# Optimization experiments

Hardware: AMD Instinct MI355X
Metric: run time of the kernel (lower is better)

## Reference

```python
import jax, jax.numpy as jnp
import numpy as np

B, N, D, V, Y = 4, 4096, 512, 50257, 16000

def setup_inputs() -> dict:
    key = jax.random.key(0)
    ks = jax.random.split(key, 5)
    # token ids in [1, V): avoid pad_id=0 so no attention row is fully -inf
    M_s = jax.random.randint(ks[0], (B, N), 1, V)
    E_v = jax.random.normal(ks[1], (V, D), jnp.float32) * 0.02
    E_y = jax.random.normal(ks[2], (Y, D), jnp.float32) * 0.02
    s = 1.0 / np.sqrt(D)  # kaiming_uniform(a=sqrt(5)) bound for [D,D]
    W_A = jax.random.uniform(ks[3], (D, D), jnp.float32, minval=-s, maxval=s)
    W_O = jax.random.uniform(ks[4], (D, D), jnp.float32, minval=-s, maxval=s)
    gamma = jnp.ones((D,), jnp.float32)
    beta = jnp.zeros((D,), jnp.float32)
    return {"M_s": M_s, "E_v": E_v, "E_y": E_y, "W_A": W_A, "W_O": W_O,
            "gamma": gamma, "beta": beta}

def _layer_norm(x, g, b, eps=1e-5):
    mu = jnp.mean(x, axis=-1, keepdims=True)
    var = jnp.mean(jnp.square(x - mu), axis=-1, keepdims=True)
    return (x - mu) * jax.lax.rsqrt(var + eps) * g + b

def reference(M_s, E_v, E_y, W_A, W_O, gamma, beta):
    # Self-attention branch (v_q=None), dropout in eval mode (identity).
    X = E_v[M_s]                                   # [B, N, D]
    mask = (M_s != 0)                              # [B, N] padding mask
    # logits = (X @ W_A) @ X^T
    logits = jnp.einsum('bnd,de,bme->bnm', X, W_A, X)   # [B, N, N]
    logits = jnp.where(mask[:, None, :], logits, -jnp.inf)
    # positional + causal bias: D = -|i-j| with future (i<j) set to -inf
    i = jnp.arange(N, dtype=jnp.float32)[:, None]
    j = jnp.arange(N, dtype=jnp.float32)[None, :]
    dist = i - j
    bias = jnp.where(dist >= 0, -dist, -jnp.inf)        # [N, N]
    A = jax.nn.softmax(logits + bias, axis=-1)          # [B, N, N]
    Q_c = jnp.einsum('bnm,bmd,de->bne', A, X, W_O)      # [B, N, D]
    H = _layer_norm(Q_c + X, gamma, beta)               # [B, N, D]
    y_logits = jnp.einsum('bnd,yd->bny', H, E_y)        # [B, N, Y]
    return y_logits, A
```

## Files before the change

kernel.cpp:

```cpp
#include <hip/hip_runtime.h>


#define DEVINL __device__ __forceinline__

typedef __attribute__((ext_vector_type(8))) short bf16x8;
typedef __attribute__((ext_vector_type(4))) float f32x4;
typedef unsigned short u16;

#define BB 4
#define NN 4096
#define DD 512
#define YY 16000
#define YPAD 16128
#define ROWS (BB * NN)

DEVINL u16 f2bf(float x) {
  unsigned u = __float_as_uint(x);
  return (u16)((u + 0x7fffu + ((u >> 16) & 1u)) >> 16);
}

DEVINL float bf2f(u16 h) { return __uint_as_float((unsigned)h << 16); }

DEVINL void gload16(const void* g, void* l) {
  __builtin_amdgcn_global_load_lds(
      (const __attribute__((address_space(1))) void*)g,
      (__attribute__((address_space(3))) void*)l, 16, 0, 0);
}

DEVINL void zero_acc(f32x4 acc[4][4]) {
#pragma unroll
  for (int m = 0; m < 4; ++m)
#pragma unroll
    for (int n = 0; n < 4; ++n) {
      acc[m][n][0] = 0.f; acc[m][n][1] = 0.f;
      acc[m][n][2] = 0.f; acc[m][n][3] = 0.f;
    }
}

DEVINL void gemm_bt_core(const u16* __restrict__ A, int lda,
                         const u16* __restrict__ Bm, int ldb, int ksteps,
                         u16* sA, u16* sB, f32x4 acc[4][4], int tid) {
  const int lane = tid & 63, w = tid >> 6;
  const int wr = (w >> 1) * 64, wc = (w & 1) * 64;
  const int c0 = w * 128 + lane, c1 = c0 + 64;
  const u16* gA0 = A + (size_t)(c0 >> 2) * lda + (c0 & 3) * 8;
  const u16* gA1 = A + (size_t)(c1 >> 2) * lda + (c1 & 3) * 8;
  const u16* gB0 = Bm + (size_t)(c0 >> 2) * ldb + (c0 & 3) * 8;
  const u16* gB1 = Bm + (size_t)(c1 >> 2) * ldb + (c1 & 3) * 8;
  u16* lA0 = sA + w * 1024;  u16* lA1 = lA0 + 512;
  u16* lB0 = sB + w * 1024;  u16* lB1 = lB0 + 512;
  const int fr = lane & 15, fk = (lane >> 4) * 8;

  for (int kt = 0; kt < ksteps; ++kt) {
    __syncthreads();
    gload16(gA0 + kt * 32, lA0);
    gload16(gA1 + kt * 32, lA1);
    gload16(gB0 + kt * 32, lB0);
    gload16(gB1 + kt * 32, lB1);
    __syncthreads();
    bf16x8 af[4], bfv[4];
#pragma unroll
    for (int m = 0; m < 4; ++m)
      af[m] = *(const bf16x8*)(sA + (wr + m * 16 + fr) * 32 + fk);
#pragma unroll
    for (int n = 0; n < 4; ++n)
      bfv[n] = *(const bf16x8*)(sB + (wc + n * 16 + fr) * 32 + fk);
#pragma unroll
    for (int m = 0; m < 4; ++m)
#pragma unroll
      for (int n = 0; n < 4; ++n)
        acc[m][n] = __builtin_amdgcn_mfma_f32_16x16x32_bf16(af[m], bfv[n],
                                                            acc[m][n], 0, 0, 0);
  }
}

#define C256_STAGE(kt, buf)                                    \
  {                                                            \
    const u16* a0 = Ag + (kt) * 64;                            \
    const u16* b0 = Bg + (kt) * 64;                            \
    u16* Lb = lds + (buf) * 32768;                             \
    gload16(a0 + offE0, Lb + d0);                              \
    gload16(a0 + offE1, Lb + d1);                              \
    gload16(a0 + 65536 + offE0, Lb + 8192 + d0);               \
    gload16(a0 + 65536 + offE1, Lb + 8192 + d1);               \
    gload16(b0 + offE0, Lb + 16384 + d0);                      \
    gload16(b0 + offE1, Lb + 16384 + d1);                      \
    gload16(b0 + 65536 + offE0, Lb + 24576 + d0);              \
    gload16(b0 + 65536 + offE1, Lb + 24576 + d1);              \
  }

DEVINL void core256(const u16* __restrict__ Ag, const u16* __restrict__ Bg,
                    u16* lds, f32x4 (&acc)[8][4], int tid) {
  const int lane = tid & 63, w = tid >> 6;
  const int wm = w >> 2, wn = w & 3;

  int offE0, offE1;
  {
    int q = tid;
    int r = (((q >> 6) >> 1) << 4) | ((q >> 2) & 15);
    int c = (((q >> 6) & 1) << 5) |
            (((q & 3) << 3) ^ (((q >> 5) & 1) << 4) ^ (((q >> 4) & 1) << 3));
    offE0 = r * DD + c;
    q = 512 + tid;
    r = (((q >> 6) >> 1) << 4) | ((q >> 2) & 15);
    c = (((q >> 6) & 1) << 5) |
        (((q & 3) << 3) ^ (((q >> 5) & 1) << 4) ^ (((q >> 4) & 1) << 3));
    offE1 = r * DD + c;
  }
  const int d0 = w * 512, d1 = 4096 + w * 512;

  int x = (lane & 15) * 64 + ((lane >> 4) & 3) * 16;
  int fxu = (x ^ (((x >> 9) & 1) << 5) ^ (((x >> 8) & 1) << 4)) >> 1;

#pragma unroll
  for (int m = 0; m < 8; ++m)
#pragma unroll
    for (int n = 0; n < 4; ++n) {
      acc[m][n][0] = 0.f; acc[m][n][1] = 0.f;
      acc[m][n][2] = 0.f; acc[m][n][3] = 0.f;
    }

  C256_STAGE(0, 0);
  C256_STAGE(1, 1);
  asm volatile("s_waitcnt vmcnt(8)" ::: "memory");
  __syncthreads();

  for (int c = 0; c < 8; ++c) {
    const u16* L = lds + (c & 1) * 32768;
    const u16* pa = L + wm * 8192;
    const u16* pb = L + 16384 + (wn >> 1) * 8192 + (wn & 1) * 4096;
    bf16x8 af[4][2], bf[4][2];
#pragma unroll
    for (int n = 0; n < 2; ++n)
#pragma unroll
      for (int ks = 0; ks < 2; ++ks)
        bf[n][ks] = *(const bf16x8*)(pb + (n * 2 + ks) * 512 + fxu);
#pragma unroll
    for (int m = 0; m < 4; ++m)
#pragma unroll
      for (int ks = 0; ks < 2; ++ks)
        af[m][ks] = *(const bf16x8*)(pa + (m * 2 + ks) * 512 + fxu);
    __builtin_amdgcn_s_setprio(1);
#pragma unroll
    for (int m = 0; m < 4; ++m)
#pragma unroll
      for (int n = 0; n < 2; ++n)
#pragma unroll
        for (int ks = 0; ks < 2; ++ks)
          acc[m][n] = __builtin_amdgcn_mfma_f32_16x16x32_bf16(
              af[m][ks], bf[n][ks], acc[m][n], 0, 0, 0);
    __builtin_amdgcn_s_setprio(0);
#pragma unroll
    for (int n = 2; n < 4; ++n)
#pragma unroll
      for (int ks = 0; ks < 2; ++ks)
        bf[n][ks] = *(const bf16x8*)(pb + (n * 2 + ks) * 512 + fxu);
    __builtin_amdgcn_s_setprio(1);
#pragma unroll
    for (int m = 0; m < 4; ++m)
#pragma unroll
      for (int n = 2; n < 4; ++n)
#pragma unroll
        for (int ks = 0; ks < 2; ++ks)
          acc[m][n] = __builtin_amdgcn_mfma_f32_16x16x32_bf16(
              af[m][ks], bf[n][ks], acc[m][n], 0, 0, 0);
    __builtin_amdgcn_s_setprio(0);
#pragma unroll
    for (int m = 0; m < 4; ++m)
#pragma unroll
      for (int ks = 0; ks < 2; ++ks)
        af[m][ks] = *(const bf16x8*)(pa + ((m + 4) * 2 + ks) * 512 + fxu);
    __builtin_amdgcn_s_setprio(1);
#pragma unroll
    for (int m = 0; m < 4; ++m)
#pragma unroll
      for (int n = 0; n < 2; ++n)
#pragma unroll
        for (int ks = 0; ks < 2; ++ks)
          acc[m + 4][n] = __builtin_amdgcn_mfma_f32_16x16x32_bf16(
              af[m][ks], bf[n][ks], acc[m + 4][n], 0, 0, 0);
#pragma unroll
    for (int m = 0; m < 4; ++m)
#pragma unroll
      for (int n = 2; n < 4; ++n)
#pragma unroll
        for (int ks = 0; ks < 2; ++ks)
          acc[m + 4][n] = __builtin_amdgcn_mfma_f32_16x16x32_bf16(
              af[m][ks], bf[n][ks], acc[m + 4][n], 0, 0, 0);
    __builtin_amdgcn_s_setprio(0);

    __syncthreads();
    if (c < 6) {
      C256_STAGE(c + 2, c & 1);
      asm volatile("s_waitcnt vmcnt(8)" ::: "memory");
    } else if (c == 6) {
      asm volatile("s_waitcnt vmcnt(0)" ::: "memory");
    }
    __syncthreads();
  }
}

__global__ __launch_bounds__(128) void prep_gather(const int* __restrict__ Ms,
                                                   const float* __restrict__ Ev,
                                                   u16* __restrict__ Xb) {
  int row = blockIdx.x, tid = threadIdx.x;
  int tok = Ms[row];
  float4 v = *(const float4*)(Ev + (size_t)tok * DD + tid * 4);
  *(ushort4*)(Xb + (size_t)row * DD + tid * 4) =
      make_ushort4(f2bf(v.x), f2bf(v.y), f2bf(v.z), f2bf(v.w));
}

__global__ __launch_bounds__(256) void prep_wt(const float* __restrict__ W,
                                               u16* __restrict__ Wt) {
  __shared__ u16 t[64][65];
  int dt = blockIdx.x, et = blockIdx.y, tid = threadIdx.x;
#pragma unroll
  for (int p = 0; p < 16; ++p) {
    int e = tid + 256 * p; int r = e >> 6, c = e & 63;
    t[r][c] = f2bf(W[(size_t)(dt * 64 + r) * DD + et * 64 + c]);
  }
  __syncthreads();
#pragma unroll
  for (int p = 0; p < 16; ++p) {
    int e = tid + 256 * p; int r = e >> 6, c = e & 63;
    Wt[(size_t)(et * 64 + r) * DD + dt * 64 + c] = t[c][r];
  }
}

__global__ __launch_bounds__(256) void prep_ey(const float* __restrict__ Ey,
                                               u16* __restrict__ Eyb) {
  size_t i4 = (size_t)blockIdx.x * 256 + threadIdx.x;
  size_t row = i4 >> 7;
  ushort4 h;
  if (row < YY) {
    float4 v = *(const float4*)(Ey + i4 * 4);
    h = make_ushort4(f2bf(v.x), f2bf(v.y), f2bf(v.z), f2bf(v.w));
  } else {
    h = make_ushort4(0, 0, 0, 0);
  }
  *(ushort4*)(Eyb + i4 * 4) = h;
}

__global__ __launch_bounds__(256) void prep_xt(const u16* __restrict__ Xb,
                                               u16* __restrict__ XbT) {
  __shared__ u16 t[64][65];
  int tid = threadIdx.x;
  int nt = blockIdx.x, dt = blockIdx.y, b = blockIdx.z;
  const u16* src = Xb + ((size_t)b * NN + nt * 64) * DD + dt * 64;
#pragma unroll
  for (int p = 0; p < 16; ++p) {
    int e = tid + 256 * p; int r = e >> 6, c = e & 63;
    t[r][c] = src[(size_t)r * DD + c];
  }
  __syncthreads();
  u16* dst = XbT + ((size_t)b * DD + dt * 64) * NN + nt * 64;
#pragma unroll
  for (int p = 0; p < 16; ++p) {
    int e = tid + 256 * p; int r = e >> 6, c = e & 63;
    dst[(size_t)r * NN + c] = t[c][r];
  }
}

__global__ __launch_bounds__(256) void k2_xw(const u16* __restrict__ Xb,
                                             const u16* __restrict__ WAt,
                                             u16* __restrict__ XWb) {
  __shared__ u16 sA[4096], sB[4096];
  f32x4 acc[4][4]; zero_acc(acc);
  int tid = threadIdx.x;
  size_t row0 = (size_t)blockIdx.x * 128, col0 = (size_t)blockIdx.y * 128;
  gemm_bt_core(Xb + row0 * DD, DD, WAt + col0 * DD, DD, DD / 32, sA, sB, acc, tid);
  int lane = tid & 63, w = tid >> 6;
  int wr = (w >> 1) * 64, wc = (w & 1) * 64;
  int cr = (lane >> 4) * 4, cc = lane & 15;
#pragma unroll
  for (int m = 0; m < 4; ++m)
#pragma unroll
    for (int n = 0; n < 4; ++n)
#pragma unroll
      for (int r = 0; r < 4; ++r) {
        size_t gi = row0 + wr + m * 16 + cr + r;
        size_t gj = col0 + wc + n * 16 + cc;
        XWb[gi * DD + gj] = f2bf(acc[m][n][r]);
      }
}

__global__ __launch_bounds__(256) void k3_scores(const u16* __restrict__ XWb,
                                                 const u16* __restrict__ Xb,
                                                 u16* __restrict__ Ebf) {
  int t = blockIdx.x, b = blockIdx.z;
  int ib = (int)((sqrtf(8.f * (float)t + 1.f) - 1.f) * 0.5f);
  while ((ib + 1) * (ib + 2) / 2 <= t) ++ib;
  while (ib * (ib + 1) / 2 > t) --ib;
  int jb = t - ib * (ib + 1) / 2;
  __shared__ u16 sA[4096], sB[4096];
  f32x4 acc[4][4]; zero_acc(acc);
  int tid = threadIdx.x;
  const u16* Ap = XWb + ((size_t)b * NN + ib * 128) * DD;
  const u16* Bp = Xb  + ((size_t)b * NN + jb * 128) * DD;
  gemm_bt_core(Ap, DD, Bp, DD, DD / 32, sA, sB, acc, tid);
  int lane = tid & 63, w = tid >> 6;
  int wr = (w >> 1) * 64, wc = (w & 1) * 64;
  int cr = (lane >> 4) * 4, cc = lane & 15;
  u16* Eb = Ebf + (size_t)b * NN * NN;
#pragma unroll
  for (int m = 0; m < 4; ++m)
#pragma unroll
    for (int n = 0; n < 4; ++n)
#pragma unroll
      for (int r = 0; r < 4; ++r) {
        int i = ib * 128 + wr + m * 16 + cr + r;
        int j = jb * 128 + wc + n * 16 + cc;
        float e = (j > i) ? 0.f : __expf(acc[m][n][r] - (float)(i - j));
        Eb[(size_t)i * NN + j] = f2bf(e);
      }
}

__global__ __launch_bounds__(256) void k4_softmax(const u16* __restrict__ Ebf,
                                                  float* __restrict__ Aout,
                                                  float* __restrict__ invb) {
  __shared__ u16 srow[NN];
  __shared__ float red[4];
  size_t row = blockIdx.x;
  int i = (int)(row & (NN - 1));
  const u16* E = Ebf + row * (size_t)NN;
  float* S = Aout + row * (size_t)NN;
  int len = i + 1, tid = threadIdx.x;
  int padend = (len + 127) & ~127;
  int nc = padend >> 3;
  for (int v = tid; v < nc; v += 256)
    *(uint4*)(srow + v * 8) = *(const uint4*)(E + v * 8);
  __syncthreads();
  float l = 0.f;
  for (int v = tid; v < nc; v += 256) {
    uint4 x = *(const uint4*)(srow + v * 8);
    l += bf2f((u16)(x.x & 0xffff)) + bf2f((u16)(x.x >> 16));
    l += bf2f((u16)(x.y & 0xffff)) + bf2f((u16)(x.y >> 16));
    l += bf2f((u16)(x.z & 0xffff)) + bf2f((u16)(x.z >> 16));
    l += bf2f((u16)(x.w & 0xffff)) + bf2f((u16)(x.w >> 16));
  }
#pragma unroll
  for (int o = 32; o; o >>= 1) l += __shfl_xor(l, o);
  if ((tid & 63) == 0) red[tid >> 6] = l;
  __syncthreads();
  float inv = 1.f / (red[0] + red[1] + red[2] + red[3]);
  if (tid == 0) invb[row] = inv;
  for (int v = tid; v < NN / 4; v += 256) {
    int k = v * 4;
    float4 a = make_float4(0.f, 0.f, 0.f, 0.f);
    if (k < padend) {
      ushort4 e = *(const ushort4*)(srow + k);
      a = make_float4(bf2f(e.x) * inv, bf2f(e.y) * inv,
                      bf2f(e.z) * inv, bf2f(e.w) * inv);
    }
    *(float4*)(S + k) = a;
  }
}

__global__ __launch_bounds__(256) void k5_ax(const u16* __restrict__ Ebf,
                                             const u16* __restrict__ XbT,
                                             const float* __restrict__ invb,
                                             u16* __restrict__ AXb) {
  int u = blockIdx.x;
  int half = u >> 8, v = u & 255;
  int ib = v & 31; if (half) ib = 31 - ib;
  int db = (v >> 5) & 3;
  int b = (half << 1) | (v >> 7);
  __shared__ u16 sA[4096], sB[4096];
  f32x4 acc[4][4]; zero_acc(acc);
  int tid = threadIdx.x;
  const u16* Ap = Ebf + ((size_t)b * NN + ib * 128) * NN;
  const u16* Bp = XbT + ((size_t)b * DD + db * 128) * NN;
  gemm_bt_core(Ap, NN, Bp, NN, (ib + 1) * 4, sA, sB, acc, tid);
  int lane = tid & 63, w = tid >> 6;
  int wr = (w >> 1) * 64, wc = (w & 1) * 64;
  int cr = (lane >> 4) * 4, cc = lane & 15;
#pragma unroll
  for (int m = 0; m < 4; ++m)
#pragma unroll
    for (int r = 0; r < 4; ++r) {
      int i = ib * 128 + wr + m * 16 + cr + r;
      float sc = invb[(size_t)b * NN + i];
#pragma unroll
      for (int n = 0; n < 4; ++n) {
        int d = db * 128 + wc + n * 16 + cc;
        AXb[((size_t)b * NN + i) * DD + d] = f2bf(acc[m][n][r] * sc);
      }
    }
}

__global__ __launch_bounds__(256) void k6_qc(const u16* __restrict__ AXb,
                                             const u16* __restrict__ WOt,
                                             float* __restrict__ Qc32) {
  __shared__ u16 sA[4096], sB[4096];
  f32x4 acc[4][4]; zero_acc(acc);
  int tid = threadIdx.x;
  size_t row0 = (size_t)blockIdx.x * 128, col0 = (size_t)blockIdx.y * 128;
  gemm_bt_core(AXb + row0 * DD, DD, WOt + col0 * DD, DD, DD / 32, sA, sB, acc, tid);
  int lane = tid & 63, w = tid >> 6;
  int wr = (w >> 1) * 64, wc = (w & 1) * 64;
  int cr = (lane >> 4) * 4, cc = lane & 15;
#pragma unroll
  for (int m = 0; m < 4; ++m)
#pragma unroll
    for (int n = 0; n < 4; ++n)
#pragma unroll
      for (int r = 0; r < 4; ++r) {
        size_t gi = row0 + wr + m * 16 + cr + r;
        size_t gj = col0 + wc + n * 16 + cc;
        Qc32[gi * DD + gj] = acc[m][n][r];
      }
}

__global__ __launch_bounds__(128) void k6b_ln(const float* __restrict__ Qc,
                                              const u16* __restrict__ Xb,
                                              const float* __restrict__ gamma,
                                              const float* __restrict__ beta,
                                              u16* __restrict__ Hb) {
  int row = blockIdx.x, tid = threadIdx.x;
  float4 q = *(const float4*)(Qc + (size_t)row * DD + tid * 4);
  ushort4 xu = *(const ushort4*)(Xb + (size_t)row * DD + tid * 4);
  float v0 = q.x + bf2f(xu.x), v1 = q.y + bf2f(xu.y);
  float v2 = q.z + bf2f(xu.z), v3 = q.w + bf2f(xu.w);
  float s = v0 + v1 + v2 + v3;
  float s2 = v0 * v0 + v1 * v1 + v2 * v2 + v3 * v3;
#pragma unroll
  for (int o = 32; o; o >>= 1) { s += __shfl_xor(s, o); s2 += __shfl_xor(s2, o); }
  __shared__ float r1[2], r2[2];
  int lane = tid & 63, w = tid >> 6;
  if (lane == 0) { r1[w] = s; r2[w] = s2; }
  __syncthreads();
  s = r1[0] + r1[1]; s2 = r2[0] + r2[1];
  float mu = s * (1.f / 512.f);
  float var = s2 * (1.f / 512.f) - mu * mu;
  float rs = 1.f / sqrtf(var + 1e-5f);
  float4 g  = *(const float4*)(gamma + tid * 4);
  float4 be = *(const float4*)(beta + tid * 4);
  ushort4 h = make_ushort4(f2bf((v0 - mu) * rs * g.x + be.x),
                           f2bf((v1 - mu) * rs * g.y + be.y),
                           f2bf((v2 - mu) * rs * g.z + be.z),
                           f2bf((v3 - mu) * rs * g.w + be.w));
  *(ushort4*)(Hb + (size_t)row * DD + tid * 4) = h;
}

__global__ __launch_bounds__(512, 2) void k7_logits(const u16* __restrict__ Hb,
                                                    const u16* __restrict__ Eyb,
                                                    float* __restrict__ Yout) {
  __shared__ u16 lds[65536];
  const int tid = threadIdx.x;
  const int lane = tid & 63, w = tid >> 6;
  const int wm = w >> 2, wn = w & 3;

  int id = blockIdx.x;
  int swz = (id & 7) * (4032 / 8) + (id >> 3);
  size_t row0 = (size_t)(swz & 63) * 256;
  size_t col0 = (size_t)(swz >> 6) * 256;

  f32x4 acc[8][4];
  core256(Hb + row0 * DD, Eyb + col0 * DD, lds, acc, tid);

  const int cr = (lane >> 4) * 4, cc = lane & 15;
#pragma unroll
  for (int m = 0; m < 8; ++m)
#pragma unroll
    for (int n = 0; n < 4; ++n) {
      size_t gj = col0 + wn * 64 + n * 16 + cc;
      if (gj < YY) {
        size_t gi = row0 + wm * 128 + m * 16 + cr;
#pragma unroll
        for (int rr = 0; rr < 4; ++rr)
          Yout[(gi + rr) * (size_t)YY + gj] = acc[m][n][rr];
      }
    }
}

extern "C" void kernel_launch(void* const* d_in, const int* in_sizes, int n_in,
                              void* d_out, int out_size, void* d_ws, size_t ws_size,
                              hipStream_t stream) {
  (void)in_sizes; (void)n_in; (void)out_size; (void)ws_size;
  const int*   Ms    = (const int*)d_in[0];
  const float* Ev    = (const float*)d_in[1];
  const float* Ey    = (const float*)d_in[2];
  const float* WA    = (const float*)d_in[3];
  const float* WO    = (const float*)d_in[4];
  const float* gamma = (const float*)d_in[5];
  const float* beta  = (const float*)d_in[6];

  float* Yout = (float*)d_out;
  float* Aout = Yout + (size_t)BB * NN * YY;

  char* w = (char*)d_ws;
  u16* Xb  = (u16*)w; w += (size_t)ROWS * DD * 2;
  u16* XbT = (u16*)w; w += (size_t)BB * DD * NN * 2;
  u16* XWb = (u16*)w; w += (size_t)ROWS * DD * 2;
  u16* AXb = (u16*)w; w += (size_t)ROWS * DD * 2;
  u16* Hb  = (u16*)w; w += (size_t)ROWS * DD * 2;
  u16* WAt = (u16*)w; w += (size_t)DD * DD * 2;
  u16* WOt = (u16*)w; w += (size_t)DD * DD * 2;
  u16* Eyb = (u16*)w; w += (size_t)YPAD * DD * 2;
  u16* Ebf = (u16*)w; w += (size_t)ROWS * NN * 2;
  float* invb = (float*)w; w += (size_t)ROWS * 4;
  float* Qc32 = (float*)XbT;

  prep_gather<<<ROWS, 128, 0, stream>>>(Ms, Ev, Xb);
  prep_wt<<<dim3(8, 8), 256, 0, stream>>>(WA, WAt);
  prep_wt<<<dim3(8, 8), 256, 0, stream>>>(WO, WOt);
  prep_ey<<<YPAD * DD / 4 / 256, 256, 0, stream>>>(Ey, Eyb);
  prep_xt<<<dim3(NN / 64, DD / 64, BB), 256, 0, stream>>>(Xb, XbT);
  k2_xw<<<dim3(ROWS / 128, DD / 128), 256, 0, stream>>>(Xb, WAt, XWb);
  k3_scores<<<dim3(528, 1, BB), 256, 0, stream>>>(XWb, Xb, Ebf);
  k4_softmax<<<ROWS, 256, 0, stream>>>(Ebf, Aout, invb);
  k5_ax<<<512, 256, 0, stream>>>(Ebf, XbT, invb, AXb);
  k6_qc<<<dim3(ROWS / 128, DD / 128), 256, 0, stream>>>(AXb, WOt, Qc32);
  k6b_ln<<<ROWS, 128, 0, stream>>>(Qc32, Xb, gamma, beta, Hb);
  k7_logits<<<dim3(64 * 63), 512, 0, stream>>>(Hb, Eyb, Yout);
}
```

Baseline: 860.3 us.

## Defer softmax normalization into LayerNorm, store Qc as bf16, merge prep kernels

The 1/rowsum softmax normalization moves out of the AX GEMM epilogue and into the LayerNorm kernel, using the identity that diag(inv)·(AX)·W_O = diag(inv)·(AX·W_O). This frees k5 and k6 from depending on k4_softmax, so they now run before it. The W_O GEMM output is written as bf16 into the dead XWb buffer instead of fp32, halving that intermediate's write and read traffic at the cost of extra rounding before normalization. The gather, weight-transpose and E_y conversion prep kernels are merged into a single launch to cut launch overhead.

```diff
diff --git a/kernel.cpp b/kernel.cpp
--- a/kernel.cpp
+++ b/kernel.cpp
@@ -200,45 +200,53 @@
   }
 }
 
-__global__ __launch_bounds__(128) void prep_gather(const int* __restrict__ Ms,
-                                                   const float* __restrict__ Ev,
-                                                   u16* __restrict__ Xb) {
-  int row = blockIdx.x, tid = threadIdx.x;
-  int tok = Ms[row];
-  float4 v = *(const float4*)(Ev + (size_t)tok * DD + tid * 4);
-  *(ushort4*)(Xb + (size_t)row * DD + tid * 4) =
-      make_ushort4(f2bf(v.x), f2bf(v.y), f2bf(v.z), f2bf(v.w));
-}
-
-__global__ __launch_bounds__(256) void prep_wt(const float* __restrict__ W,
-                                               u16* __restrict__ Wt) {
+__global__ __launch_bounds__(256) void prep_all(const int* __restrict__ Ms,
+                                                const float* __restrict__ Ev,
+                                                const float* __restrict__ WA,
+                                                const float* __restrict__ WO,
+                                                const float* __restrict__ Ey,
+                                                u16* __restrict__ Xb,
+                                                u16* __restrict__ WAt,
+                                                u16* __restrict__ WOt,
+                                                u16* __restrict__ Eyb) {
   __shared__ u16 t[64][65];
-  int dt = blockIdx.x, et = blockIdx.y, tid = threadIdx.x;
-#pragma unroll
-  for (int p = 0; p < 16; ++p) {
-    int e = tid + 256 * p; int r = e >> 6, c = e & 63;
-    t[r][c] = f2bf(W[(size_t)(dt * 64 + r) * DD + et * 64 + c]);
-  }
-  __syncthreads();
-#pragma unroll
-  for (int p = 0; p < 16; ++p) {
-    int e = tid + 256 * p; int r = e >> 6, c = e & 63;
-    Wt[(size_t)(et * 64 + r) * DD + dt * 64 + c] = t[c][r];
-  }
-}
-
-__global__ __launch_bounds__(256) void prep_ey(const float* __restrict__ Ey,
-                                               u16* __restrict__ Eyb) {
-  size_t i4 = (size_t)blockIdx.x * 256 + threadIdx.x;
-  size_t row = i4 >> 7;
-  ushort4 h;
-  if (row < YY) {
-    float4 v = *(const float4*)(Ey + i4 * 4);
-    h = make_ushort4(f2bf(v.x), f2bf(v.y), f2bf(v.z), f2bf(v.w));
+  int bx = blockIdx.x, tid = threadIdx.x;
+  if (bx < 8192) {
+    int row = bx * 2 + (tid >> 7);
+    int t4 = tid & 127;
+    int tok = Ms[row];
+    float4 v = *(const float4*)(Ev + (size_t)tok * DD + t4 * 4);
+    *(ushort4*)(Xb + (size_t)row * DD + t4 * 4) =
+        make_ushort4(f2bf(v.x), f2bf(v.y), f2bf(v.z), f2bf(v.w));
+  } else if (bx < 8320) {
+    int k = bx - 8192;
+    const float* W = (k < 64) ? WA : WO;
+    u16* Wt = (k < 64) ? WAt : WOt;
+    k &= 63;
+    int dt = k >> 3, et = k & 7;
+#pragma unroll
+    for (int p = 0; p < 16; ++p) {
+      int e = tid + 256 * p; int r = e >> 6, c = e & 63;
+      t[r][c] = f2bf(W[(size_t)(dt * 64 + r) * DD + et * 64 + c]);
+    }
+    __syncthreads();
+#pragma unroll
+    for (int p = 0; p < 16; ++p) {
+      int e = tid + 256 * p; int r = e >> 6, c = e & 63;
+      Wt[(size_t)(et * 64 + r) * DD + dt * 64 + c] = t[c][r];
+    }
   } else {
-    h = make_ushort4(0, 0, 0, 0);
-  }
-  *(ushort4*)(Eyb + i4 * 4) = h;
+    size_t i4 = (size_t)(bx - 8320) * 256 + tid;
+    size_t row = i4 >> 7;
+    ushort4 h;
+    if (row < YY) {
+      float4 v = *(const float4*)(Ey + i4 * 4);
+      h = make_ushort4(f2bf(v.x), f2bf(v.y), f2bf(v.z), f2bf(v.w));
+    } else {
+      h = make_ushort4(0, 0, 0, 0);
+    }
+    *(ushort4*)(Eyb + i4 * 4) = h;
+  }
 }
 
 __global__ __launch_bounds__(256) void prep_xt(const u16* __restrict__ Xb,
@@ -312,6 +320,58 @@
         int j = jb * 128 + wc + n * 16 + cc;
         float e = (j > i) ? 0.f : __expf(acc[m][n][r] - (float)(i - j));
         Eb[(size_t)i * NN + j] = f2bf(e);
+      }
+}
+
+__global__ __launch_bounds__(256) void k5_ax(const u16* __restrict__ Ebf,
+                                             const u16* __restrict__ XbT,
+                                             u16* __restrict__ AXb) {
+  int u = blockIdx.x;
+  int half = u >> 8, v = u & 255;
+  int ib = v & 31; if (half) ib = 31 - ib;
+  int db = (v >> 5) & 3;
+  int b = (half << 1) | (v >> 7);
+  __shared__ u16 sA[4096], sB[4096];
+  f32x4 acc[4][4]; zero_acc(acc);
+  int tid = threadIdx.x;
+  const u16* Ap = Ebf + ((size_t)b * NN + ib * 128) * NN;
+  const u16* Bp = XbT + ((size_t)b * DD + db * 128) * NN;
+  gemm_bt_core(Ap, NN, Bp, NN, (ib + 1) * 4, sA, sB, acc, tid);
+  int lane = tid & 63, w = tid >> 6;
+  int wr = (w >> 1) * 64, wc = (w & 1) * 64;
+  int cr = (lane >> 4) * 4, cc = lane & 15;
+#pragma unroll
+  for (int m = 0; m < 4; ++m)
+#pragma unroll
+    for (int n = 0; n < 4; ++n)
+#pragma unroll
+      for (int r = 0; r < 4; ++r) {
+        int i = ib * 128 + wr + m * 16 + cr + r;
+        int d = db * 128 + wc + n * 16 + cc;
+        AXb[((size_t)b * NN + i) * DD + d] = f2bf(acc[m][n][r]);
+      }
+}
+
+__global__ __launch_bounds__(256) void k6_qc(const u16* __restrict__ AXb,
+                                             const u16* __restrict__ WOt,
+                                             u16* __restrict__ Qcb) {
+  __shared__ u16 sA[4096], sB[4096];
+  f32x4 acc[4][4]; zero_acc(acc);
+  int tid = threadIdx.x;
+  size_t row0 = (size_t)blockIdx.x * 128, col0 = (size_t)blockIdx.y * 128;
+  gemm_bt_core(AXb + row0 * DD, DD, WOt + col0 * DD, DD, DD / 32, sA, sB, acc, tid);
+  int lane = tid & 63, w = tid >> 6;
+  int wr = (w >> 1) * 64, wc = (w & 1) * 64;
+  int cr = (lane >> 4) * 4, cc = lane & 15;
+#pragma unroll
+  for (int m = 0; m < 4; ++m)
+#pragma unroll
+    for (int n = 0; n < 4; ++n)
+#pragma unroll
+      for (int r = 0; r < 4; ++r) {
+        size_t gi = row0 + wr + m * 16 + cr + r;
+        size_t gj = col0 + wc + n * 16 + cc;
+        Qcb[gi * DD + gj] = f2bf(acc[m][n][r]);
       }
 }
 
@@ -356,71 +416,18 @@
   }
 }
 
-__global__ __launch_bounds__(256) void k5_ax(const u16* __restrict__ Ebf,
-                                             const u16* __restrict__ XbT,
-                                             const float* __restrict__ invb,
-                                             u16* __restrict__ AXb) {
-  int u = blockIdx.x;
-  int half = u >> 8, v = u & 255;
-  int ib = v & 31; if (half) ib = 31 - ib;
-  int db = (v >> 5) & 3;
-  int b = (half << 1) | (v >> 7);
-  __shared__ u16 sA[4096], sB[4096];
-  f32x4 acc[4][4]; zero_acc(acc);
-  int tid = threadIdx.x;
-  const u16* Ap = Ebf + ((size_t)b * NN + ib * 128) * NN;
-  const u16* Bp = XbT + ((size_t)b * DD + db * 128) * NN;
-  gemm_bt_core(Ap, NN, Bp, NN, (ib + 1) * 4, sA, sB, acc, tid);
-  int lane = tid & 63, w = tid >> 6;
-  int wr = (w >> 1) * 64, wc = (w & 1) * 64;
-  int cr = (lane >> 4) * 4, cc = lane & 15;
-#pragma unroll
-  for (int m = 0; m < 4; ++m)
-#pragma unroll
-    for (int r = 0; r < 4; ++r) {
-      int i = ib * 128 + wr + m * 16 + cr + r;
-      float sc = invb[(size_t)b * NN + i];
-#pragma unroll
-      for (int n = 0; n < 4; ++n) {
-        int d = db * 128 + wc + n * 16 + cc;
-        AXb[((size_t)b * NN + i) * DD + d] = f2bf(acc[m][n][r] * sc);
-      }
-    }
-}
-
-__global__ __launch_bounds__(256) void k6_qc(const u16* __restrict__ AXb,
-                                             const u16* __restrict__ WOt,
-                                             float* __restrict__ Qc32) {
-  __shared__ u16 sA[4096], sB[4096];
-  f32x4 acc[4][4]; zero_acc(acc);
-  int tid = threadIdx.x;
-  size_t row0 = (size_t)blockIdx.x * 128, col0 = (size_t)blockIdx.y * 128;
-  gemm_bt_core(AXb + row0 * DD, DD, WOt + col0 * DD, DD, DD / 32, sA, sB, acc, tid);
-  int lane = tid & 63, w = tid >> 6;
-  int wr = (w >> 1) * 64, wc = (w & 1) * 64;
-  int cr = (lane >> 4) * 4, cc = lane & 15;
-#pragma unroll
-  for (int m = 0; m < 4; ++m)
-#pragma unroll
-    for (int n = 0; n < 4; ++n)
-#pragma unroll
-      for (int r = 0; r < 4; ++r) {
-        size_t gi = row0 + wr + m * 16 + cr + r;
-        size_t gj = col0 + wc + n * 16 + cc;
-        Qc32[gi * DD + gj] = acc[m][n][r];
-      }
-}
-
-__global__ __launch_bounds__(128) void k6b_ln(const float* __restrict__ Qc,
+__global__ __launch_bounds__(128) void k6b_ln(const u16* __restrict__ Qcb,
                                               const u16* __restrict__ Xb,
+                                              const float* __restrict__ invb,
                                               const float* __restrict__ gamma,
                                               const float* __restrict__ beta,
                                               u16* __restrict__ Hb) {
   int row = blockIdx.x, tid = threadIdx.x;
-  float4 q = *(const float4*)(Qc + (size_t)row * DD + tid * 4);
+  float inv = invb[row];
+  ushort4 qu = *(const ushort4*)(Qcb + (size_t)row * DD + tid * 4);
   ushort4 xu = *(const ushort4*)(Xb + (size_t)row * DD + tid * 4);
-  float v0 = q.x + bf2f(xu.x), v1 = q.y + bf2f(xu.y);
-  float v2 = q.z + bf2f(xu.z), v3 = q.w + bf2f(xu.w);
+  float v0 = bf2f(qu.x) * inv + bf2f(xu.x), v1 = bf2f(qu.y) * inv + bf2f(xu.y);
+  float v2 = bf2f(qu.z) * inv + bf2f(xu.z), v3 = bf2f(qu.w) * inv + bf2f(xu.w);
   float s = v0 + v1 + v2 + v3;
   float s2 = v0 * v0 + v1 * v1 + v2 * v2 + v3 * v3;
 #pragma unroll
@@ -499,18 +506,15 @@
   u16* Eyb = (u16*)w; w += (size_t)YPAD * DD * 2;
   u16* Ebf = (u16*)w; w += (size_t)ROWS * NN * 2;
   float* invb = (float*)w; w += (size_t)ROWS * 4;
-  float* Qc32 = (float*)XbT;
-
-  prep_gather<<<ROWS, 128, 0, stream>>>(Ms, Ev, Xb);
-  prep_wt<<<dim3(8, 8), 256, 0, stream>>>(WA, WAt);
-  prep_wt<<<dim3(8, 8), 256, 0, stream>>>(WO, WOt);
-  prep_ey<<<YPAD * DD / 4 / 256, 256, 0, stream>>>(Ey, Eyb);
+  u16* Qcb = XWb;
+
+  prep_all<<<16384, 256, 0, stream>>>(Ms, Ev, WA, WO, Ey, Xb, WAt, WOt, Eyb);
   prep_xt<<<dim3(NN / 64, DD / 64, BB), 256, 0, stream>>>(Xb, XbT);
   k2_xw<<<dim3(ROWS / 128, DD / 128), 256, 0, stream>>>(Xb, WAt, XWb);
   k3_scores<<<dim3(528, 1, BB), 256, 0, stream>>>(XWb, Xb, Ebf);
+  k5_ax<<<512, 256, 0, stream>>>(Ebf, XbT, AXb);
+  k6_qc<<<dim3(ROWS / 128, DD / 128), 256, 0, stream>>>(AXb, WOt, Qcb);
   k4_softmax<<<ROWS, 256, 0, stream>>>(Ebf, Aout, invb);
-  k5_ax<<<512, 256, 0, stream>>>(Ebf, XbT, invb, AXb);
-  k6_qc<<<dim3(ROWS / 128, DD / 128), 256, 0, stream>>>(AXb, WOt, Qc32);
-  k6b_ln<<<ROWS, 128, 0, stream>>>(Qc32, Xb, gamma, beta, Hb);
+  k6b_ln<<<ROWS, 128, 0, stream>>>(Qcb, Xb, invb, gamma, beta, Hb);
   k7_logits<<<dim3(64 * 63), 512, 0, stream>>>(Hb, Eyb, Yout);
 }
```

New measurement: 820.5 us. 4.6% less time.
